# Optimization experiments

Measured on AMD Instinct MI355X. Metric: run time of the kernel, lower is better.

The kernel has to match this reference:

```python
import jax, jax.numpy as jnp
import numpy as np

EMBED_DIM = 1024
NUM_HEADS = 16
HEAD_DIM = EMBED_DIM // NUM_HEADS


def setup_inputs() -> dict:
    key = jax.random.key(0)
    ks = jax.random.split(key, 5)
    B, N = 4, 2048
    s_in = 1.0 / np.sqrt(EMBED_DIM)
    return {
        "x": jax.random.normal(ks[0], (B, N, EMBED_DIM), dtype=jnp.float32),
        "qkv_w": jax.random.uniform(ks[1], (3 * EMBED_DIM, EMBED_DIM), jnp.float32, -s_in, s_in),
        "qkv_b": jax.random.uniform(ks[2], (3 * EMBED_DIM,), jnp.float32, -s_in, s_in),
        "o_w": jax.random.uniform(ks[3], (EMBED_DIM, EMBED_DIM), jnp.float32, -s_in, s_in),
        "o_b": jax.random.uniform(ks[4], (EMBED_DIM,), jnp.float32, -s_in, s_in),
    }


def reference(x, qkv_w, qkv_b, o_w, o_b):
    B, N, E = x.shape
    H, D = NUM_HEADS, HEAD_DIM
    # qkv: [B, N, 3E] -> [B, N, H, 3D] -> [B, H, N, 3D], then chunk last dim
    qkv = (jnp.einsum('bne,fe->bnf', x, qkv_w) + qkv_b)
    qkv = qkv.reshape(B, N, H, 3 * D).transpose(0, 2, 1, 3)
    q, k, v = jnp.split(qkv, 3, axis=-1)
    scale = 1.0 / np.sqrt(D)
    scores = jnp.einsum('bhqd,bhkd->bhqk', q, k) * scale
    attn = jax.nn.softmax(scores, axis=-1)  # dropout is identity in eval mode
    out = jnp.einsum('bhqk,bhkd->bhqd', attn, v)
    out = out.transpose(0, 2, 1, 3).reshape(B, N, E)
    return jnp.einsum('bne,fe->bnf', out, o_w) + o_b
```

## Files before the change

### kernel.cpp

```cpp
#include <hip/hip_runtime.h>

typedef unsigned short u16;
typedef float f32x4 __attribute__((ext_vector_type(4)));
typedef float f32x16 __attribute__((ext_vector_type(16)));
typedef short bf16x8 __attribute__((ext_vector_type(8)));
typedef int i32x2 __attribute__((ext_vector_type(2)));

__device__ __forceinline__ u16 f2bf(float f){
  union { float f; unsigned u; } x; x.f = f;
  unsigned r = (x.u + 0x7FFFu + ((x.u >> 16) & 1u)) >> 16;
  return (u16)r;
}

__device__ __forceinline__ unsigned cvtpk(float lo, float hi){
  unsigned r;
  asm("v_cvt_pk_bf16_f32 %0, %1, %2" : "=v"(r) : "v"(lo), "v"(hi));
  return r;
}

__device__ __forceinline__ void exp4q(float& a, float& b, float& c, float& d){
  asm("v_exp_f32 %0, %0\n\t"
      "v_exp_f32 %1, %1\n\t"
      "v_exp_f32 %2, %2\n\t"
      "v_exp_f32 %3, %3\n\t"
      "s_nop 1"
      : "+v"(a), "+v"(b), "+v"(c), "+v"(d));
}

__device__ __forceinline__ f32x4 mfma_bf16(bf16x8 a, bf16x8 b, f32x4 c){
  return __builtin_amdgcn_mfma_f32_16x16x32_bf16(a, b, c, 0, 0, 0);
}

__device__ __forceinline__ f32x16 mfma32(bf16x8 a, bf16x8 b, f32x16 c){
  return __builtin_amdgcn_mfma_f32_32x32x16_bf16(a, b, c, 0, 0, 0);
}

__device__ __forceinline__ void gload16(const u16* g, u16* l){
  __builtin_amdgcn_global_load_lds((__attribute__((address_space(1))) void*)g,
                                   (__attribute__((address_space(3))) void*)l, 16, 0, 0);
}

__global__ void cvt_all(const float* __restrict__ x, const float* __restrict__ w1,
                        const float* __restrict__ w2,
                        u16* __restrict__ ox, u16* __restrict__ o1, u16* __restrict__ o2,
                        int nx4, int n14, int n24){
  int stride = gridDim.x * blockDim.x;
  int ntot = nx4 + n14 + n24;
  for (int i = blockIdx.x*blockDim.x + threadIdx.x; i < ntot; i += stride){
    const float* src; u16* dst; int j = i;
    if (j < nx4){ src = x; dst = ox; }
    else if (j < nx4 + n14){ j -= nx4; src = w1; dst = o1; }
    else { j -= nx4 + n14; src = w2; dst = o2; }
    float4 v = ((const float4*)src)[j];
    ushort4 o;
    o.x = f2bf(v.x); o.y = f2bf(v.y); o.z = f2bf(v.z); o.w = f2bf(v.w);
    ((ushort4*)dst)[j] = o;
  }
}

template<int NCH, int NTHR>
__device__ __forceinline__ void stage32(const u16* src, int ld, u16* lds, int tid){
#pragma unroll
  for (int i = 0; i < NCH/NTHR; i++){
    int c = i*NTHR + tid;
    int row = c >> 2, slot = c & 3;
    int col = ((slot ^ (row & 3)) << 3);
    gload16(src + (size_t)row*ld + col, lds + ((size_t)(c & ~63) << 3));
  }
}

template<int NTHR>
__device__ __forceinline__ void stage64(const u16* src, int ld, u16* lds, int tid){
#pragma unroll
  for (int i = 0; i < 512/NTHR; i++){
    int c = i*NTHR + tid;
    int row = c >> 3, slot = c & 7;
    int col = ((slot ^ (row & 7)) << 3);
    gload16(src + (size_t)row*ld + col, lds + ((size_t)(c & ~63) << 3));
  }
}

__launch_bounds__(256)
__global__ void gemm_bt1(const u16* __restrict__ A, const u16* __restrict__ Bw,
                         const float* __restrict__ bias, float* __restrict__ Co,
                         int M, int Nf, int K)
{
  __shared__ u16 lsA[2][128*32];
  __shared__ u16 lsB[2][128*32];
  int tid = threadIdx.x;
  int wave = tid >> 6, lane = tid & 63, grp = lane >> 4, l16 = lane & 15;
  int ntn = Nf >> 7;
  int bm = blockIdx.x / ntn, bn = blockIdx.x % ntn;
  const u16* Ab = A + (size_t)bm*128*K;
  const u16* Bb = Bw + (size_t)bn*128*K;
  int wm = wave >> 1, wn = wave & 1;
  f32x4 acc[4][4] = {};

  stage32<512,256>(Ab, K, lsA[0], tid);
  stage32<512,256>(Bb, K, lsB[0], tid);
  int nk = K >> 5;
  for (int t = 0; t < nk; t++){
    __syncthreads();
    int cur = t & 1;
    if (t + 1 < nk){
      stage32<512,256>(Ab + ((t+1) << 5), K, lsA[cur^1], tid);
      stage32<512,256>(Bb + ((t+1) << 5), K, lsB[cur^1], tid);
    }
    const u16* la = lsA[cur];
    const u16* lb = lsB[cur];
    bf16x8 af[4], bfr[4];
#pragma unroll
    for (int mf = 0; mf < 4; mf++){
      int row = wm*64 + mf*16 + l16;
      af[mf] = *(const bf16x8*)(la + row*32 + ((grp ^ (row & 3)) << 3));
    }
#pragma unroll
    for (int nf = 0; nf < 4; nf++){
      int row = wn*64 + nf*16 + l16;
      bfr[nf] = *(const bf16x8*)(lb + row*32 + ((grp ^ (row & 3)) << 3));
    }
#pragma unroll
    for (int mf = 0; mf < 4; mf++)
#pragma unroll
      for (int nf = 0; nf < 4; nf++)
        acc[mf][nf] = mfma_bf16(af[mf], bfr[nf], acc[mf][nf]);
  }

  int mrow0 = bm*128 + wm*64;
  int f0 = bn*128 + wn*64;
#pragma unroll
  for (int nf = 0; nf < 4; nf++){
    int f = f0 + nf*16 + l16;
    float bv = bias[f];
#pragma unroll
    for (int mf = 0; mf < 4; mf++){
      int mbase = mrow0 + mf*16 + grp*4;
#pragma unroll
      for (int r = 0; r < 4; r++)
        Co[(size_t)(mbase + r)*Nf + f] = acc[mf][nf][r] + bv;
    }
  }
}

__launch_bounds__(512, 1)
__global__ void gemm_qkv(const u16* __restrict__ A, const u16* __restrict__ Bw,
                         const float* __restrict__ bias,
                         u16* __restrict__ Qp, u16* __restrict__ Kp,
                         u16* __restrict__ Vt, int M, int Nf, int K)
{
  __shared__ u16 lsA[2][256*64];
  __shared__ u16 lsB[2][256*64];
  int tid = threadIdx.x;
  int lane = tid & 63, grp = lane >> 4, l16 = lane & 15;
  int wave = tid >> 6;
  int wr = wave >> 2, wc = wave & 3;
  int ntn = Nf >> 8;
  int bid = (blockIdx.x & 7) * 48 + (blockIdx.x >> 3);
  int bm = bid / ntn, bn = bid % ntn;
  const u16* Ab = A + (size_t)bm*256*K;
  const u16* Bb = Bw + (size_t)bn*256*K;

  f32x4 acc[8][4] = {};

  auto stageHalf = [&](const u16* src, u16* lds, int h){
#pragma unroll
    for (int i = 0; i < 2; i++){
      int c = i*512 + tid;
      int row = h*128 + (c >> 3);
      int col = (((c & 7) ^ (row & 7)) << 3);
      gload16(src + (size_t)row*K + col, lds + h*8192 + ((size_t)(c & ~63) << 3));
    }
  };

  stageHalf(Ab, lsA[0], 0);
  stageHalf(Bb, lsB[0], 0);
  stageHalf(Ab, lsA[0], 1);
  stageHalf(Bb, lsB[0], 1);
  asm volatile("s_waitcnt vmcnt(4)" ::: "memory");

  int nkt = K >> 6;
  for (int t = 0; t < nkt; t++){
    const u16* la = lsA[t & 1];
    const u16* lb = lsB[t & 1];
    const u16* As = Ab + ((t+1) << 6);
    const u16* Bs = Bb + ((t+1) << 6);
    u16* dA = lsA[(t+1) & 1];
    u16* dB = lsB[(t+1) & 1];
    bool pf = (t + 1) < nkt;
    bf16x8 af[4][2], bf[2][2];

    __builtin_amdgcn_s_barrier();
#pragma unroll
    for (int m = 0; m < 4; m++){
      int grow = (m*2 + wr)*16 + l16;
#pragma unroll
      for (int ks = 0; ks < 2; ks++)
        af[m][ks] = *(const bf16x8*)(la + grow*64 + (((ks*4+grp) ^ (grow & 7)) << 3));
    }
#pragma unroll
    for (int n = 0; n < 2; n++){
      int brow = (n*4 + wc)*16 + l16;
#pragma unroll
      for (int ks = 0; ks < 2; ks++)
        bf[n][ks] = *(const bf16x8*)(lb + brow*64 + (((ks*4+grp) ^ (brow & 7)) << 3));
    }
    if (pf) stageHalf(As, dA, 0);
    __builtin_amdgcn_s_setprio(1);
#pragma unroll
    for (int m = 0; m < 4; m++)
#pragma unroll
      for (int n = 0; n < 2; n++)
#pragma unroll
        for (int ks = 0; ks < 2; ks++)
          acc[m][n] = mfma_bf16(af[m][ks], bf[n][ks], acc[m][n]);
    __builtin_amdgcn_s_setprio(0);
    if (pf) asm volatile("s_waitcnt vmcnt(4)" ::: "memory");
    else    asm volatile("s_waitcnt vmcnt(2)" ::: "memory");

    __builtin_amdgcn_s_barrier();
#pragma unroll
    for (int m = 0; m < 4; m++){
      int grow = ((m+4)*2 + wr)*16 + l16;
#pragma unroll
      for (int ks = 0; ks < 2; ks++)
        af[m][ks] = *(const bf16x8*)(la + grow*64 + (((ks*4+grp) ^ (grow & 7)) << 3));
    }
    if (pf) stageHalf(Bs, dB, 0);
    __builtin_amdgcn_s_setprio(1);
#pragma unroll
    for (int m = 0; m < 4; m++)
#pragma unroll
      for (int n = 0; n < 2; n++)
#pragma unroll
        for (int ks = 0; ks < 2; ks++)
          acc[m+4][n] = mfma_bf16(af[m][ks], bf[n][ks], acc[m+4][n]);
    __builtin_amdgcn_s_setprio(0);
    if (pf) asm volatile("s_waitcnt vmcnt(4)" ::: "memory");
    else    asm volatile("s_waitcnt vmcnt(0)" ::: "memory");

    __builtin_amdgcn_s_barrier();
#pragma unroll
    for (int n = 0; n < 2; n++){
      int brow = ((n+2)*4 + wc)*16 + l16;
#pragma unroll
      for (int ks = 0; ks < 2; ks++)
        bf[n][ks] = *(const bf16x8*)(lb + brow*64 + (((ks*4+grp) ^ (brow & 7)) << 3));
    }
    if (pf) stageHalf(As, dA, 1);
    __builtin_amdgcn_s_setprio(1);
#pragma unroll
    for (int m = 0; m < 4; m++)
#pragma unroll
      for (int n = 0; n < 2; n++)
#pragma unroll
        for (int ks = 0; ks < 2; ks++)
          acc[m+4][n+2] = mfma_bf16(af[m][ks], bf[n][ks], acc[m+4][n+2]);
    __builtin_amdgcn_s_setprio(0);

#pragma unroll
    for (int m = 0; m < 4; m++){
      int grow = (m*2 + wr)*16 + l16;
#pragma unroll
      for (int ks = 0; ks < 2; ks++)
        af[m][ks] = *(const bf16x8*)(la + grow*64 + (((ks*4+grp) ^ (grow & 7)) << 3));
    }
    if (pf) stageHalf(Bs, dB, 1);
    __builtin_amdgcn_s_setprio(1);
#pragma unroll
    for (int m = 0; m < 4; m++)
#pragma unroll
      for (int n = 0; n < 2; n++)
#pragma unroll
        for (int ks = 0; ks < 2; ks++)
          acc[m][n+2] = mfma_bf16(af[m][ks], bf[n][ks], acc[m][n+2]);
    __builtin_amdgcn_s_setprio(0);
    if (pf) asm volatile("s_waitcnt vmcnt(4)" ::: "memory");
  }

#pragma unroll
  for (int n = 0; n < 4; n++){
    int f = bn*256 + (n*4 + wc)*16 + l16;
    float bv = bias[f];
    int h = f / 192, c = f % 192;
#pragma unroll
    for (int m = 0; m < 8; m++){
      int mbase = bm*256 + (m*2 + wr)*16 + grp*4;
      int bb = mbase >> 11, n0 = mbase & 2047;
      size_t bh = (size_t)bb*16 + h;
      if (c >= 128){
        ushort4 w;
        w.x = f2bf(acc[m][n][0] + bv);
        w.y = f2bf(acc[m][n][1] + bv);
        w.z = f2bf(acc[m][n][2] + bv);
        w.w = f2bf(acc[m][n][3] + bv);
        *(ushort4*)(Vt + (bh*64 + (size_t)(c - 128))*2048 + n0) = w;
      } else {
        u16* dst = (c < 64) ? Qp : Kp;
        float sc = (c < 64) ? 0.18033688011f : 1.0f;
        int cc = c & 63;
#pragma unroll
        for (int r = 0; r < 4; r++)
          dst[(bh*2048 + n0 + r)*64 + cc] = f2bf((acc[m][n][r] + bv) * sc);
      }
    }
  }
}

__device__ __forceinline__ bf16x8 packP(const f32x16& pp, int base){
  unsigned t0 = cvtpk(pp[base+0], pp[base+1]);
  unsigned t1 = cvtpk(pp[base+2], pp[base+3]);
  unsigned t2 = cvtpk(pp[base+4], pp[base+5]);
  unsigned t3 = cvtpk(pp[base+6], pp[base+7]);
  i32x2 r02 = __builtin_amdgcn_permlane32_swap((int)t0, (int)t2, false, false);
  i32x2 r13 = __builtin_amdgcn_permlane32_swap((int)t1, (int)t3, false, false);
  union { unsigned u[4]; bf16x8 v; } pu;
  pu.u[0] = (unsigned)r02.x;
  pu.u[1] = (unsigned)r13.x;
  pu.u[2] = (unsigned)r02.y;
  pu.u[3] = (unsigned)r13.y;
  return pu.v;
}

__device__ __forceinline__ void expv16(f32x16& p){
#pragma unroll
  for (int r = 0; r < 16; r += 4){
    float a = p[r], b = p[r+1], c = p[r+2], d = p[r+3];
    exp4q(a, b, c, d);
    p[r] = a; p[r+1] = b; p[r+2] = c; p[r+3] = d;
  }
}

__launch_bounds__(512, 4)
__global__ void attn_fwd(const u16* __restrict__ Qg, const u16* __restrict__ Kg,
                         const u16* __restrict__ Vtg, u16* __restrict__ Oa)
{
  __shared__ u16 kl[4][64*64];
  __shared__ u16 vl[4][64*64];
  int tid = threadIdx.x;
  int lane = tid & 63, wave = tid >> 6;
  int q32 = lane & 31, hi = lane >> 5;
  int bid = (blockIdx.x & 7) * 64 + (blockIdx.x >> 3);
  int bh = bid >> 3, qt = bid & 7;
  int b = bh >> 4, h = bh & 15;
  int q0 = qt*256 + wave*32;
  const u16* Qb = Qg + ((size_t)bh*2048 + q0)*64;
  const u16* Kb = Kg + (size_t)bh*2048*64;
  const u16* Vb = Vtg + (size_t)bh*64*2048;

  bf16x8 qf[4];
#pragma unroll
  for (int s = 0; s < 4; s++)
    qf[s] = *(const bf16x8*)(Qb + q32*64 + s*16 + hi*8);

  f32x16 lacc = {};
  f32x16 oacc[2] = {};

#pragma unroll
  for (int t = 0; t < 3; t++){
    stage64<512>(Kb + (size_t)t*64*64, 64, kl[t], tid);
    stage64<512>(Vb + t*64, 2048, vl[t], tid);
  }

  for (int kt = 0; kt < 32; kt++){
    if (kt < 30)       asm volatile("s_waitcnt vmcnt(4)" ::: "memory");
    else if (kt == 30) asm volatile("s_waitcnt vmcnt(2)" ::: "memory");
    else               asm volatile("s_waitcnt vmcnt(0)" ::: "memory");
    __builtin_amdgcn_s_barrier();
    __builtin_amdgcn_sched_barrier(0);
    if (kt + 3 < 32){
      stage64<512>(Kb + (size_t)(kt+3)*64*64, 64, kl[(kt+3)&3], tid);
      stage64<512>(Vb + (kt+3)*64, 2048, vl[(kt+3)&3], tid);
    }
    const u16* lk = kl[kt & 3];
    const u16* lv = vl[kt & 3];

    f32x16 p0 = {}, p1 = {};
    __builtin_amdgcn_s_setprio(1);
#pragma unroll
    for (int s = 0; s < 4; s++){
      int r0 = q32;
      bf16x8 k0 = *(const bf16x8*)(lk + r0*64 + (((s*2+hi) ^ (r0 & 7)) << 3));
      p0 = mfma32(k0, qf[s], p0);
      int r1 = 32 + q32;
      bf16x8 k1 = *(const bf16x8*)(lk + r1*64 + (((s*2+hi) ^ (r1 & 7)) << 3));
      p1 = mfma32(k1, qf[s], p1);
    }
    __builtin_amdgcn_s_setprio(0);

    expv16(p0); expv16(p1);
#pragma unroll
    for (int r = 0; r < 16; r++) lacc[r] += p0[r];
#pragma unroll
    for (int r = 0; r < 16; r++) lacc[r] += p1[r];

#pragma unroll
    for (int ks = 0; ks < 4; ks++){
      bf16x8 pb = packP((ks < 2) ? p0 : p1, (ks & 1) * 8);
      __builtin_amdgcn_s_setprio(1);
      int rowd0 = q32;
      bf16x8 v0 = *(const bf16x8*)(lv + rowd0*64 + (((ks*2+hi) ^ (rowd0 & 7)) << 3));
      oacc[0] = mfma32(v0, pb, oacc[0]);
      int rowd1 = 32 + q32;
      bf16x8 v1 = *(const bf16x8*)(lv + rowd1*64 + (((ks*2+hi) ^ (rowd1 & 7)) << 3));
      oacc[1] = mfma32(v1, pb, oacc[1]);
      __builtin_amdgcn_s_setprio(0);
    }
  }

#pragma unroll
  for (int r = 0; r < 8; r++) lacc[r] += lacc[r+8];
#pragma unroll
  for (int r = 0; r < 4; r++) lacc[r] += lacc[r+4];
  float l = (lacc[0] + lacc[1]) + (lacc[2] + lacc[3]);
  l += __shfl_xor(l, 32, 64);
  float inv = 1.0f / l;

  size_t obase = ((size_t)b*2048 + q0 + q32)*1024 + h*64;
#pragma unroll
  for (int dblk = 0; dblk < 2; dblk++)
#pragma unroll
    for (int rb = 0; rb < 4; rb++){
      ushort4 w;
      w.x = f2bf(oacc[dblk][rb*4+0] * inv);
      w.y = f2bf(oacc[dblk][rb*4+1] * inv);
      w.z = f2bf(oacc[dblk][rb*4+2] * inv);
      w.w = f2bf(oacc[dblk][rb*4+3] * inv);
      *(ushort4*)(Oa + obase + dblk*32 + rb*8 + hi*4) = w;
    }
}

extern "C" void kernel_launch(void* const* d_in, const int* in_sizes, int n_in,
                              void* d_out, int out_size, void* d_ws, size_t ws_size,
                              hipStream_t stream)
{
  const float* x    = (const float*)d_in[0];
  const float* qkvw = (const float*)d_in[1];
  const float* qkvb = (const float*)d_in[2];
  const float* ow   = (const float*)d_in[3];
  const float* ob   = (const float*)d_in[4];
  float* out = (float*)d_out;

  u16* xb = (u16*)d_ws;
  u16* wq = xb + (size_t)8192*1024;
  u16* wo = wq + (size_t)3072*1024;
  u16* Qp = wo + (size_t)1024*1024;
  u16* Kp = Qp + (size_t)64*2048*64;
  u16* Vt = Kp + (size_t)64*2048*64;
  u16* Oa = Vt + (size_t)64*2048*64;

  cvt_all<<<2048, 256, 0, stream>>>(x, qkvw, ow, xb, wq, wo,
                                    (8192*1024)/4, (3072*1024)/4, (1024*1024)/4);

  gemm_qkv<<<32*12, 512, 0, stream>>>(xb, wq, qkvb, Qp, Kp, Vt, 8192, 3072, 1024);
  attn_fwd<<<512, 512, 0, stream>>>(Qp, Kp, Vt, Oa);
  gemm_bt1<<<64*8, 256, 0, stream>>>(Oa, wo, ob, out, 8192, 1024, 1024);
}
```

Measured before the change: 190.5 us.

## Restructure QKV GEMM main loop into 8-phase ping-pong schedule with explicit barriers

Rewrites the QKV projection GEMM main loop to process two K-tiles per iteration in eight quarter phases. Each phase reads LDS fragments, issues part of the next global-to-LDS stage, then waits on a barrier and lgkmcnt before the MFMA block. Prefetch is deepened by staging parts of the second tile in the prologue. The aim is tighter overlap of global loads, LDS reads and MFMAs, at the cost of more barriers per tile and a more fragile ordering of the double-buffer halves.

```diff
diff --git a/kernel.cpp b/kernel.cpp
--- a/kernel.cpp
+++ b/kernel.cpp
@@ -171,111 +171,110 @@
       gload16(src + (size_t)row*K + col, lds + h*8192 + ((size_t)(c & ~63) << 3));
     }
   };
+  auto readA = [&](const u16* la, int mo, bf16x8 (&af)[4][2]){
+#pragma unroll
+    for (int m = 0; m < 4; m++){
+      int grow = ((m+mo)*2 + wr)*16 + l16;
+#pragma unroll
+      for (int ks = 0; ks < 2; ks++)
+        af[m][ks] = *(const bf16x8*)(la + grow*64 + (((ks*4+grp) ^ (grow & 7)) << 3));
+    }
+  };
+  auto readB = [&](const u16* lb, int no, bf16x8 (&bf)[2][2]){
+#pragma unroll
+    for (int n = 0; n < 2; n++){
+      int brow = ((n+no)*4 + wc)*16 + l16;
+#pragma unroll
+      for (int ks = 0; ks < 2; ks++)
+        bf[n][ks] = *(const bf16x8*)(lb + brow*64 + (((ks*4+grp) ^ (brow & 7)) << 3));
+    }
+  };
+  auto mmaQ = [&](bf16x8 (&af)[4][2], bf16x8 (&bf)[2][2], int mo, int no){
+    __builtin_amdgcn_s_setprio(1);
+#pragma unroll
+    for (int m = 0; m < 4; m++)
+#pragma unroll
+      for (int n = 0; n < 2; n++)
+#pragma unroll
+        for (int ks = 0; ks < 2; ks++)
+          acc[m+mo][n+no] = mfma_bf16(af[m][ks], bf[n][ks], acc[m+mo][n+no]);
+    __builtin_amdgcn_s_setprio(0);
+  };
+#define QBAR() asm volatile("s_barrier" ::: "memory")
+#define QLGKM() asm volatile("s_waitcnt lgkmcnt(0)" ::: "memory")
 
   stageHalf(Ab, lsA[0], 0);
   stageHalf(Bb, lsB[0], 0);
   stageHalf(Ab, lsA[0], 1);
   stageHalf(Bb, lsB[0], 1);
+  stageHalf(Bb + (1 << 6), lsB[1], 0);
+  stageHalf(Ab + (1 << 6), lsA[1], 1);
   asm volatile("s_waitcnt vmcnt(4)" ::: "memory");
-
-  int nkt = K >> 6;
-  for (int t = 0; t < nkt; t++){
-    const u16* la = lsA[t & 1];
-    const u16* lb = lsB[t & 1];
-    const u16* As = Ab + ((t+1) << 6);
-    const u16* Bs = Bb + ((t+1) << 6);
-    u16* dA = lsA[(t+1) & 1];
-    u16* dB = lsB[(t+1) & 1];
-    bool pf = (t + 1) < nkt;
+  QBAR();
+
+  int nit = K >> 7;
+  for (int j = 0; j < nit; j++){
+    const u16* la0 = lsA[0];
+    const u16* lb0 = lsB[0];
+    const u16* la1 = lsA[1];
+    const u16* lb1 = lsB[1];
+    int t1 = 2*j + 1, t2 = 2*j + 2, t3 = 2*j + 3;
+    bool pf = (j < nit - 1);
     bf16x8 af[4][2], bf[2][2];
 
-    __builtin_amdgcn_s_barrier();
-#pragma unroll
-    for (int m = 0; m < 4; m++){
-      int grow = (m*2 + wr)*16 + l16;
-#pragma unroll
-      for (int ks = 0; ks < 2; ks++)
-        af[m][ks] = *(const bf16x8*)(la + grow*64 + (((ks*4+grp) ^ (grow & 7)) << 3));
-    }
-#pragma unroll
-    for (int n = 0; n < 2; n++){
-      int brow = (n*4 + wc)*16 + l16;
-#pragma unroll
-      for (int ks = 0; ks < 2; ks++)
-        bf[n][ks] = *(const bf16x8*)(lb + brow*64 + (((ks*4+grp) ^ (brow & 7)) << 3));
-    }
-    if (pf) stageHalf(As, dA, 0);
-    __builtin_amdgcn_s_setprio(1);
-#pragma unroll
-    for (int m = 0; m < 4; m++)
-#pragma unroll
-      for (int n = 0; n < 2; n++)
-#pragma unroll
-        for (int ks = 0; ks < 2; ks++)
-          acc[m][n] = mfma_bf16(af[m][ks], bf[n][ks], acc[m][n]);
-    __builtin_amdgcn_s_setprio(0);
-    if (pf) asm volatile("s_waitcnt vmcnt(4)" ::: "memory");
-    else    asm volatile("s_waitcnt vmcnt(2)" ::: "memory");
-
-    __builtin_amdgcn_s_barrier();
-#pragma unroll
-    for (int m = 0; m < 4; m++){
-      int grow = ((m+4)*2 + wr)*16 + l16;
-#pragma unroll
-      for (int ks = 0; ks < 2; ks++)
-        af[m][ks] = *(const bf16x8*)(la + grow*64 + (((ks*4+grp) ^ (grow & 7)) << 3));
-    }
-    if (pf) stageHalf(Bs, dB, 0);
-    __builtin_amdgcn_s_setprio(1);
-#pragma unroll
-    for (int m = 0; m < 4; m++)
-#pragma unroll
-      for (int n = 0; n < 2; n++)
-#pragma unroll
-        for (int ks = 0; ks < 2; ks++)
-          acc[m+4][n] = mfma_bf16(af[m][ks], bf[n][ks], acc[m+4][n]);
-    __builtin_amdgcn_s_setprio(0);
+    readA(la0, 0, af); readB(lb0, 0, bf);
+    stageHalf(Ab + (t1 << 6), lsA[1], 0);
+    QBAR(); QLGKM();
+    mmaQ(af, bf, 0, 0);
+    QBAR();
+
+    readA(la0, 4, af);
+    stageHalf(Bb + (t1 << 6), lsB[1], 1);
+    QBAR(); QLGKM();
+    mmaQ(af, bf, 4, 0);
+    QBAR();
+
+    readB(lb0, 2, bf);
+    if (pf) stageHalf(Bb + (t2 << 6), lsB[0], 0);
+    QBAR(); QLGKM();
+    mmaQ(af, bf, 4, 2);
+    QBAR();
+
+    readA(la0, 0, af);
+    if (pf) stageHalf(Ab + (t2 << 6), lsA[0], 1);
+    QBAR(); QLGKM();
+    mmaQ(af, bf, 0, 2);
     if (pf) asm volatile("s_waitcnt vmcnt(4)" ::: "memory");
     else    asm volatile("s_waitcnt vmcnt(0)" ::: "memory");
-
-    __builtin_amdgcn_s_barrier();
-#pragma unroll
-    for (int n = 0; n < 2; n++){
-      int brow = ((n+2)*4 + wc)*16 + l16;
-#pragma unroll
-      for (int ks = 0; ks < 2; ks++)
-        bf[n][ks] = *(const bf16x8*)(lb + brow*64 + (((ks*4+grp) ^ (brow & 7)) << 3));
-    }
-    if (pf) stageHalf(As, dA, 1);
-    __builtin_amdgcn_s_setprio(1);
-#pragma unroll
-    for (int m = 0; m < 4; m++)
-#pragma unroll
-      for (int n = 0; n < 2; n++)
-#pragma unroll
-        for (int ks = 0; ks < 2; ks++)
-          acc[m+4][n+2] = mfma_bf16(af[m][ks], bf[n][ks], acc[m+4][n+2]);
-    __builtin_amdgcn_s_setprio(0);
-
-#pragma unroll
-    for (int m = 0; m < 4; m++){
-      int grow = (m*2 + wr)*16 + l16;
-#pragma unroll
-      for (int ks = 0; ks < 2; ks++)
-        af[m][ks] = *(const bf16x8*)(la + grow*64 + (((ks*4+grp) ^ (grow & 7)) << 3));
-    }
-    if (pf) stageHalf(Bs, dB, 1);
-    __builtin_amdgcn_s_setprio(1);
-#pragma unroll
-    for (int m = 0; m < 4; m++)
-#pragma unroll
-      for (int n = 0; n < 2; n++)
-#pragma unroll
-        for (int ks = 0; ks < 2; ks++)
-          acc[m][n+2] = mfma_bf16(af[m][ks], bf[n][ks], acc[m][n+2]);
-    __builtin_amdgcn_s_setprio(0);
+    QBAR();
+
+    readA(la1, 0, af); readB(lb1, 0, bf);
+    if (pf) stageHalf(Ab + (t2 << 6), lsA[0], 0);
+    QBAR(); QLGKM();
+    mmaQ(af, bf, 0, 0);
+    QBAR();
+
+    readA(la1, 4, af);
+    if (pf) stageHalf(Bb + (t2 << 6), lsB[0], 1);
+    QBAR(); QLGKM();
+    mmaQ(af, bf, 4, 0);
+    QBAR();
+
+    readB(lb1, 2, bf);
+    if (pf) stageHalf(Bb + (t3 << 6), lsB[1], 0);
+    QBAR(); QLGKM();
+    mmaQ(af, bf, 4, 2);
+    QBAR();
+
+    readA(la1, 0, af);
+    if (pf) stageHalf(Ab + (t3 << 6), lsA[1], 1);
+    QBAR(); QLGKM();
+    mmaQ(af, bf, 0, 2);
     if (pf) asm volatile("s_waitcnt vmcnt(4)" ::: "memory");
-  }
+    QBAR();
+  }
+#undef QBAR
+#undef QLGKM
 
 #pragma unroll
   for (int n = 0; n < 4; n++){
```

New measurement: 197.1 us. 3.5% more time.
